# Optimization experiments

Hardware: AMD Instinct MI355X
Metric: run time of the kernel (lower is better)

Reference implementation:

```python
import jax, jax.numpy as jnp
import numpy as np
from jax import lax

SAMPLE_RATE = 0.25
RADIUS = 0.5
NSAMPLE = 32
MLP = [64 + 3, 64, 128]  # use_xyz adds 3 to first width


def setup_inputs() -> dict:
    key = jax.random.key(0)
    ks = jax.random.split(key, 8)
    B, N, C = 8, 8192, 64
    pos = jax.random.normal(ks[0], (B, N, 3), dtype=jnp.float32)
    features = jax.random.normal(ks[1], (B, C, N), dtype=jnp.float32)
    # shared MLP (1x1 Conv2d with bias, ReLU), He-scaled init
    w0 = jax.random.normal(ks[2], (MLP[1], MLP[0]), jnp.float32) * (2.0 / MLP[0]) ** 0.5
    b0 = jnp.zeros((MLP[1],), jnp.float32)
    w1 = jax.random.normal(ks[3], (MLP[1], MLP[1]), jnp.float32) * (2.0 / MLP[1]) ** 0.5
    b1 = jnp.zeros((MLP[1],), jnp.float32)
    w2 = jax.random.normal(ks[4], (MLP[2], MLP[1]), jnp.float32) * (2.0 / MLP[1]) ** 0.5
    b2 = jnp.zeros((MLP[2],), jnp.float32)
    return {"pos": pos, "features": features, "w0": w0, "b0": b0,
            "w1": w1, "b1": b1, "w2": w2, "b2": b2}


def furthest_point_sample(pos, npoint):
    """pos: (B,N,3) -> idx (B,npoint) int32, greedy FPS starting at index 0."""
    B, N, _ = pos.shape
    init_idx = jnp.zeros((B,), jnp.int32)
    init_d = jnp.full((B, N), 1e10, jnp.float32)

    def step(carry, _):
        dists, last = carry
        p_last = jnp.take_along_axis(pos, last[:, None, None], axis=1)  # (B,1,3)
        d = jnp.sum((pos - p_last) ** 2, axis=-1)                        # (B,N)
        dists = jnp.minimum(dists, d)
        nxt = jnp.argmax(dists, axis=-1).astype(jnp.int32)
        return (dists, nxt), nxt

    (_, _), rest = lax.scan(step, (init_d, init_idx), None, length=npoint - 1)
    return jnp.concatenate([init_idx[None, :], rest], axis=0).T  # (B,npoint)


def ball_query(pos, new_xyz, nsample, radius):
    """pos (B,N,3), new_xyz (B,S,3) -> idx (B,S,nsample): first nsample pts
    within radius, padded with the first hit (0 if no hit), as in PointNet2 CUDA."""
    B, N, _ = pos.shape
    d2 = jnp.sum((new_xyz[:, :, None, :] - pos[:, None, :, :]) ** 2, axis=-1)  # (B,S,N)
    cand = jnp.where(d2 < radius * radius,
                     jnp.arange(N, dtype=jnp.int32)[None, None, :], N)
    neg_top, _ = lax.top_k(-cand, nsample)     # smallest nsample indices
    idx = -neg_top                              # ascending index order
    first = idx[..., :1]
    pad = jnp.where(first == N, 0, first)
    return jnp.where(idx == N, pad, idx)


def reference(pos, features, w0, b0, w1, b1, w2, b2):
    B, N, _ = pos.shape
    npoint = int(N * SAMPLE_RATE)
    fps_idx = furthest_point_sample(pos, npoint)                         # (B,S)
    new_xyz = jax.vmap(lambda p, i: p[i])(pos, fps_idx)                  # (B,S,3)

    idx = ball_query(pos, new_xyz, NSAMPLE, RADIUS)                      # (B,S,K)
    grouped_xyz = jax.vmap(lambda p, i: p[i])(pos, idx)                  # (B,S,K,3)
    rel_xyz = grouped_xyz - new_xyz[:, :, None, :]                       # (B,S,K,3)
    grouped_feat = jax.vmap(lambda f, i: f[:, i])(features, idx)         # (B,C,S,K)
    x = jnp.concatenate([rel_xyz.transpose(0, 3, 1, 2), grouped_feat], axis=1)  # (B,3+C,S,K)

    def conv_relu(x, w, b):  # 1x1 conv + bias + ReLU
        y = jnp.einsum('oc,bcsk->bosk', w, x) + b[None, :, None, None]
        return jax.nn.relu(y)

    x = conv_relu(x, w0, b0)
    x = conv_relu(x, w1, b1)
    x = conv_relu(x, w2, b2)
    new_features = jnp.max(x, axis=-1)                                   # (B,mlp[-1],S)
    return new_xyz, new_features
```

## Files before the change

kernel.cpp:

```cpp
#include <hip/hip_runtime.h>

#define NB 8
#define NPTS 8192
#define NC_FEAT 64
#define NS 2048
#define NK 32

__device__ __forceinline__ float d2_ref(float px, float py, float pz,
                                        float qx, float qy, float qz) {
  float dx = __fsub_rn(px, qx);
  float dy = __fsub_rn(py, qy);
  float dz = __fsub_rn(pz, qz);
  return __fadd_rn(__fadd_rn(__fmul_rn(dx, dx), __fmul_rn(dy, dy)),
                   __fmul_rn(dz, dz));
}

#define DPP_KEYMAX(key, ctrl)                                                 \
  {                                                                           \
    unsigned _lo = (unsigned)__builtin_amdgcn_update_dpp(                     \
        0, (int)(unsigned)(key), (ctrl), 0xf, 0xf, true);                     \
    unsigned _hi = (unsigned)__builtin_amdgcn_update_dpp(                     \
        0, (int)(unsigned)((key) >> 32), (ctrl), 0xf, 0xf, true);             \
    unsigned long long _o = ((unsigned long long)_hi << 32) | _lo;            \
    if (_o > (key)) (key) = _o;                                               \
  }

__global__ __launch_bounds__(1024)
void k_fps_tp(const float* __restrict__ pos, const float* __restrict__ feat,
              const float* __restrict__ w0, const float* __restrict__ w1,
              const float* __restrict__ w2,
              float* __restrict__ new_xyz, float* __restrict__ featT,
              float* __restrict__ wT) {
  __shared__ __align__(16) float smem[3 * NPTS + 64];
  const int tid = threadIdx.x;

  if (blockIdx.x < NB) {
    const int b = blockIdx.x;
    float* sx = smem;
    float* sy = smem + NPTS;
    float* sz = smem + 2 * NPTS;
    unsigned long long* rk = (unsigned long long*)(smem + 3 * NPTS);

    const float* p = pos + (size_t)b * NPTS * 3;
    for (int i = tid; i < NPTS; i += 1024) {
      sx[i] = p[3 * i + 0];
      sy[i] = p[3 * i + 1];
      sz[i] = p[3 * i + 2];
    }
    __syncthreads();

    float px[8], py[8], pz[8], dist[8];
#pragma unroll
    for (int j = 0; j < 8; ++j) {
      int idx = tid * 8 + j;
      px[j] = sx[idx]; py[j] = sy[idx]; pz[j] = sz[idx];
      dist[j] = 1e10f;
    }
    if (tid == 0) {
      new_xyz[((size_t)b * NS) * 3 + 0] = sx[0];
      new_xyz[((size_t)b * NS) * 3 + 1] = sy[0];
      new_xyz[((size_t)b * NS) * 3 + 2] = sz[0];
    }

    const int lane = tid & 63;
    const int wave = tid >> 6;
    int last = 0, buf = 0;

    for (int it = 1; it < NS; ++it) {
      float qx = sx[last], qy = sy[last], qz = sz[last];
      float bd = -1.0f;
      int bj = 0;
#pragma unroll
      for (int j = 0; j < 8; ++j) {
        float d = d2_ref(px[j], py[j], pz[j], qx, qy, qz);
        float nd = fminf(dist[j], d);
        dist[j] = nd;
        if (nd > bd) { bd = nd; bj = j; }
      }
      unsigned gidx = (unsigned)(tid * 8 + bj);
      unsigned long long key =
          ((unsigned long long)__float_as_uint(bd) << 32) | (unsigned)~gidx;
      DPP_KEYMAX(key, 0x111);
      DPP_KEYMAX(key, 0x112);
      DPP_KEYMAX(key, 0x114);
      DPP_KEYMAX(key, 0x118);
      DPP_KEYMAX(key, 0x142);
      DPP_KEYMAX(key, 0x143);
      if (lane == 63) rk[buf * 16 + wave] = key;
      __syncthreads();
      key = rk[buf * 16 + (lane & 15)];
      DPP_KEYMAX(key, 0x111);
      DPP_KEYMAX(key, 0x112);
      DPP_KEYMAX(key, 0x114);
      DPP_KEYMAX(key, 0x118);
      int fi = (int)~(unsigned)__builtin_amdgcn_readlane((int)(unsigned)key, 15);
      last = fi;
      buf ^= 1;
      if (tid == 0) {
        new_xyz[((size_t)b * NS + it) * 3 + 0] = sx[fi];
        new_xyz[((size_t)b * NS + it) * 3 + 1] = sy[fi];
        new_xyz[((size_t)b * NS + it) * 3 + 2] = sz[fi];
      }
    }
  } else if (blockIdx.x < NB + NB * (NPTS / 64)) {
    const int t = blockIdx.x - NB;
    const int b = t >> 7;
    const int n0 = (t & 127) << 6;
    float* tile = smem;
    const int col = tid & 63;
    const int r0 = tid >> 6;
#pragma unroll
    for (int q = 0; q < 4; ++q) {
      int c = r0 + q * 16;
      tile[c * 65 + col] = feat[((size_t)b * NC_FEAT + c) * NPTS + n0 + col];
    }
    __syncthreads();
#pragma unroll
    for (int q = 0; q < 4; ++q) {
      int r = r0 + q * 16;
      featT[((size_t)b * NPTS + n0 + r) * 64 + col] = tile[col * 65 + r];
    }
  } else {
    for (int i = tid; i < 67 * 64; i += 1024)
      wT[i] = w0[(i & 63) * 67 + (i >> 6)];
    for (int i = tid; i < 64 * 64; i += 1024)
      wT[67 * 64 + i] = w1[(i & 63) * 64 + (i >> 6)];
    for (int i = tid; i < 64 * 128; i += 1024)
      wT[67 * 64 + 64 * 64 + i] = w2[(i & 127) * 64 + (i >> 7)];
  }
}

__global__ __launch_bounds__(256)
void k_ball(const float* __restrict__ pos, const float* __restrict__ nxyz,
            int* __restrict__ ballidx) {
  const int wid = (blockIdx.x * 256 + threadIdx.x) >> 6;
  const int lane = threadIdx.x & 63;
  const int b = wid >> 11;
  const float qx = nxyz[wid * 3 + 0];
  const float qy = nxyz[wid * 3 + 1];
  const float qz = nxyz[wid * 3 + 2];
  const float* p = pos + (size_t)b * NPTS * 3;
  int* outp = ballidx + (size_t)wid * NK;

  int cnt = 0;
  int firstidx = 0x7fffffff;
  for (int n0 = 0; n0 < NPTS; n0 += 64) {
    const int i = n0 + lane;
    float d2 = d2_ref(p[3 * i], p[3 * i + 1], p[3 * i + 2], qx, qy, qz);
    bool hit = d2 < 0.25f;
    unsigned long long mask = __ballot(hit);
    int pre = __popcll(mask & ((1ull << lane) - 1ull));
    int slot = cnt + pre;
    if (hit && slot < NK) outp[slot] = i;
    if (hit && slot == 0) firstidx = i;
    cnt += __popcll(mask);
    if (cnt >= NK) break;
  }
#pragma unroll
  for (int m = 32; m >= 1; m >>= 1)
    firstidx = min(firstidx, __shfl_xor(firstidx, m, 64));
  int pad = (firstidx == 0x7fffffff) ? 0 : firstidx;
  int start = cnt < NK ? cnt : NK;
  if (lane < NK && lane >= start) outp[lane] = pad;
}

#define MLP_FMA16(wr, xc, acc)                                   \
  _Pragma("unroll") for (int o4 = 0; o4 < 16; ++o4) {            \
    float4 w = (wr)[o4];                                         \
    (acc)[o4 * 4 + 0] = fmaf(w.x, (xc), (acc)[o4 * 4 + 0]);      \
    (acc)[o4 * 4 + 1] = fmaf(w.y, (xc), (acc)[o4 * 4 + 1]);      \
    (acc)[o4 * 4 + 2] = fmaf(w.z, (xc), (acc)[o4 * 4 + 2]);      \
    (acc)[o4 * 4 + 3] = fmaf(w.w, (xc), (acc)[o4 * 4 + 3]);      \
  }

__global__ __launch_bounds__(256)
void k_mlp(const float* __restrict__ pos, const float* __restrict__ featT,
           const float* __restrict__ wT, const float* __restrict__ b0,
           const float* __restrict__ b1, const float* __restrict__ b2,
           const int* __restrict__ ballidx, const float* __restrict__ nxyz,
           float* __restrict__ outf) {
  __shared__ float xs[64 * 256];
  const int tid = threadIdx.x;
  const int g = blockIdx.x * 256 + tid;
  const int s = (g >> 5) & (NS - 1);
  const int b = g >> 16;

  const int idx = ballidx[g];
  const float qx = nxyz[((size_t)b * NS + s) * 3 + 0];
  const float qy = nxyz[((size_t)b * NS + s) * 3 + 1];
  const float qz = nxyz[((size_t)b * NS + s) * 3 + 2];
  const float* pp = pos + ((size_t)b * NPTS + idx) * 3;
  const float x0 = __fsub_rn(pp[0], qx);
  const float x1 = __fsub_rn(pp[1], qy);
  const float x2 = __fsub_rn(pp[2], qz);

  const float4* fT = (const float4*)(featT + ((size_t)b * NPTS + idx) * 64);
#pragma unroll
  for (int c4 = 0; c4 < 16; ++c4) {
    float4 v = fT[c4];
    xs[(c4 * 4 + 0) * 256 + tid] = v.x;
    xs[(c4 * 4 + 1) * 256 + tid] = v.y;
    xs[(c4 * 4 + 2) * 256 + tid] = v.z;
    xs[(c4 * 4 + 3) * 256 + tid] = v.w;
  }

  const float* wt0 = wT;
  const float* wt1 = wT + 67 * 64;
  const float* wt2 = wT + 67 * 64 + 64 * 64;

  float acc[64];
#pragma unroll
  for (int o = 0; o < 64; ++o) acc[o] = b0[o];
  {
    const float xr0 = x0, xr1 = x1, xr2 = x2;
    const float4* wr;
    wr = (const float4*)(wt0 + 0 * 64); MLP_FMA16(wr, xr0, acc);
    wr = (const float4*)(wt0 + 1 * 64); MLP_FMA16(wr, xr1, acc);
    wr = (const float4*)(wt0 + 2 * 64); MLP_FMA16(wr, xr2, acc);
  }
  for (int c = 0; c < 64; ++c) {
    float xc = xs[c * 256 + tid];
    const float4* wr = (const float4*)(wt0 + (3 + c) * 64);
    MLP_FMA16(wr, xc, acc);
  }
#pragma unroll
  for (int o = 0; o < 64; ++o) xs[o * 256 + tid] = fmaxf(acc[o], 0.0f);

#pragma unroll
  for (int o = 0; o < 64; ++o) acc[o] = b1[o];
  for (int c = 0; c < 64; ++c) {
    float xc = xs[c * 256 + tid];
    const float4* wr = (const float4*)(wt1 + c * 64);
    MLP_FMA16(wr, xc, acc);
  }
#pragma unroll
  for (int o = 0; o < 64; ++o) xs[o * 256 + tid] = fmaxf(acc[o], 0.0f);

#pragma unroll
  for (int h = 0; h < 2; ++h) {
#pragma unroll
    for (int o = 0; o < 64; ++o) acc[o] = b2[h * 64 + o];
    for (int c = 0; c < 64; ++c) {
      float xc = xs[c * 256 + tid];
      const float4* wr = (const float4*)(wt2 + c * 128 + h * 64);
      MLP_FMA16(wr, xc, acc);
    }
#pragma unroll
    for (int o = 0; o < 64; ++o) {
      float v = fmaxf(acc[o], 0.0f);
      v = fmaxf(v, __shfl_xor(v, 16, 64));
      v = fmaxf(v, __shfl_xor(v, 8, 64));
      v = fmaxf(v, __shfl_xor(v, 4, 64));
      v = fmaxf(v, __shfl_xor(v, 2, 64));
      v = fmaxf(v, __shfl_xor(v, 1, 64));
      if ((tid & 31) == 0)
        outf[((size_t)b * 128 + h * 64 + o) * NS + s] = v;
    }
  }
}

extern "C" void kernel_launch(void* const* d_in, const int* in_sizes, int n_in,
                              void* d_out, int out_size, void* d_ws,
                              size_t ws_size, hipStream_t stream) {
  const float* pos = (const float*)d_in[0];
  const float* feat = (const float*)d_in[1];
  const float* w0 = (const float*)d_in[2];
  const float* b0 = (const float*)d_in[3];
  const float* w1 = (const float*)d_in[4];
  const float* b1 = (const float*)d_in[5];
  const float* w2 = (const float*)d_in[6];
  const float* b2 = (const float*)d_in[7];

  float* out = (float*)d_out;
  float* new_xyz = out;
  float* new_feat = out + (size_t)NB * NS * 3;

  int* ballidx = (int*)d_ws;
  float* featT = (float*)d_ws + (size_t)NB * NS * NK;
  float* wT = featT + (size_t)NB * NPTS * 64;

  hipLaunchKernelGGL(k_fps_tp, dim3(NB + NB * (NPTS / 64) + 1), dim3(1024), 0,
                     stream, pos, feat, w0, w1, w2, new_xyz, featT, wT);
  hipLaunchKernelGGL(k_ball, dim3((NB * NS) / 4), dim3(256), 0, stream, pos,
                     new_xyz, ballidx);
  hipLaunchKernelGGL(k_mlp, dim3((NB * NS * NK) / 256), dim3(256), 0, stream,
                     pos, featT, wT, b0, b1, b2, ballidx, new_xyz, new_feat);
}
```

Before: 2.588 ms.

## Split FPS from transpose, use 512 threads with packed v2f distance updates

```diff
diff --git a/kernel.cpp b/kernel.cpp
--- a/kernel.cpp
+++ b/kernel.cpp
@@ -5,6 +5,8 @@
 #define NC_FEAT 64
 #define NS 2048
 #define NK 32
+
+typedef float v2f __attribute__((ext_vector_type(2)));
 
 __device__ __forceinline__ float d2_ref(float px, float py, float pz,
                                         float qx, float qy, float qz) {
@@ -25,107 +27,126 @@
     if (_o > (key)) (key) = _o;                                               \
   }
 
-__global__ __launch_bounds__(1024)
-void k_fps_tp(const float* __restrict__ pos, const float* __restrict__ feat,
-              const float* __restrict__ w0, const float* __restrict__ w1,
-              const float* __restrict__ w2,
-              float* __restrict__ new_xyz, float* __restrict__ featT,
-              float* __restrict__ wT) {
+__global__ __launch_bounds__(512)
+void k_fps(const float* __restrict__ pos, float* __restrict__ new_xyz) {
+#pragma clang fp contract(off)
   __shared__ __align__(16) float smem[3 * NPTS + 64];
   const int tid = threadIdx.x;
-
-  if (blockIdx.x < NB) {
-    const int b = blockIdx.x;
-    float* sx = smem;
-    float* sy = smem + NPTS;
-    float* sz = smem + 2 * NPTS;
-    unsigned long long* rk = (unsigned long long*)(smem + 3 * NPTS);
-
-    const float* p = pos + (size_t)b * NPTS * 3;
-    for (int i = tid; i < NPTS; i += 1024) {
-      sx[i] = p[3 * i + 0];
-      sy[i] = p[3 * i + 1];
-      sz[i] = p[3 * i + 2];
-    }
+  const int b = blockIdx.x;
+  float* sx = smem;
+  float* sy = smem + NPTS;
+  float* sz = smem + 2 * NPTS;
+  unsigned long long* rk = (unsigned long long*)(smem + 3 * NPTS);
+
+  const float* p = pos + (size_t)b * NPTS * 3;
+  for (int i = tid; i < NPTS; i += 512) {
+    sx[i] = p[3 * i + 0];
+    sy[i] = p[3 * i + 1];
+    sz[i] = p[3 * i + 2];
+  }
+  if (tid < 32) rk[tid] = 0ull;
+  __syncthreads();
+
+  const int base = tid * 16;
+  v2f px[8], py[8], pz[8], di[8];
+#pragma unroll
+  for (int k = 0; k < 8; ++k) {
+    px[k] = (v2f){sx[base + 2 * k], sx[base + 2 * k + 1]};
+    py[k] = (v2f){sy[base + 2 * k], sy[base + 2 * k + 1]};
+    pz[k] = (v2f){sz[base + 2 * k], sz[base + 2 * k + 1]};
+    di[k] = (v2f){1e10f, 1e10f};
+  }
+  if (tid == 0) {
+    new_xyz[((size_t)b * NS) * 3 + 0] = sx[0];
+    new_xyz[((size_t)b * NS) * 3 + 1] = sy[0];
+    new_xyz[((size_t)b * NS) * 3 + 2] = sz[0];
+  }
+
+  const int lane = tid & 63;
+  const int wave = tid >> 6;
+  const unsigned nbase = ~(unsigned)base;
+  int last = 0, buf = 0;
+
+  for (int it = 1; it < NS; ++it) {
+    float qx = sx[last], qy = sy[last], qz = sz[last];
+#pragma unroll
+    for (int k = 0; k < 8; ++k) {
+      v2f dx = px[k] - qx;
+      v2f dy = py[k] - qy;
+      v2f dz = pz[k] - qz;
+      v2f d2 = (dx * dx + dy * dy) + dz * dz;
+      di[k] = __builtin_elementwise_min(di[k], d2);
+    }
+    v2f m0 = __builtin_elementwise_max(di[0], di[1]);
+    v2f m1 = __builtin_elementwise_max(di[2], di[3]);
+    v2f m2 = __builtin_elementwise_max(di[4], di[5]);
+    v2f m3 = __builtin_elementwise_max(di[6], di[7]);
+    v2f m4 = __builtin_elementwise_max(m0, m1);
+    v2f m5 = __builtin_elementwise_max(m2, m3);
+    v2f m6 = __builtin_elementwise_max(m4, m5);
+    float bd = fmaxf(m6.x, m6.y);
+    int bj = 0;
+#pragma unroll
+    for (int j = 15; j >= 0; --j) {
+      float v = (j & 1) ? di[j >> 1].y : di[j >> 1].x;
+      if (v == bd) bj = j;
+    }
+    unsigned long long key =
+        ((unsigned long long)__float_as_uint(bd) << 32) |
+        (unsigned)(nbase - (unsigned)bj);
+    DPP_KEYMAX(key, 0x111);
+    DPP_KEYMAX(key, 0x112);
+    DPP_KEYMAX(key, 0x114);
+    DPP_KEYMAX(key, 0x118);
+    DPP_KEYMAX(key, 0x142);
+    DPP_KEYMAX(key, 0x143);
+    if (lane == 63) rk[buf * 16 + wave] = key;
     __syncthreads();
-
-    float px[8], py[8], pz[8], dist[8];
-#pragma unroll
-    for (int j = 0; j < 8; ++j) {
-      int idx = tid * 8 + j;
-      px[j] = sx[idx]; py[j] = sy[idx]; pz[j] = sz[idx];
-      dist[j] = 1e10f;
-    }
+    key = rk[buf * 16 + (lane & 15)];
+    DPP_KEYMAX(key, 0x111);
+    DPP_KEYMAX(key, 0x112);
+    DPP_KEYMAX(key, 0x114);
+    DPP_KEYMAX(key, 0x118);
+    int fi = (int)~(unsigned)__builtin_amdgcn_readlane((int)(unsigned)key, 15);
+    last = fi;
+    buf ^= 1;
     if (tid == 0) {
-      new_xyz[((size_t)b * NS) * 3 + 0] = sx[0];
-      new_xyz[((size_t)b * NS) * 3 + 1] = sy[0];
-      new_xyz[((size_t)b * NS) * 3 + 2] = sz[0];
-    }
-
-    const int lane = tid & 63;
-    const int wave = tid >> 6;
-    int last = 0, buf = 0;
-
-    for (int it = 1; it < NS; ++it) {
-      float qx = sx[last], qy = sy[last], qz = sz[last];
-      float bd = -1.0f;
-      int bj = 0;
-#pragma unroll
-      for (int j = 0; j < 8; ++j) {
-        float d = d2_ref(px[j], py[j], pz[j], qx, qy, qz);
-        float nd = fminf(dist[j], d);
-        dist[j] = nd;
-        if (nd > bd) { bd = nd; bj = j; }
-      }
-      unsigned gidx = (unsigned)(tid * 8 + bj);
-      unsigned long long key =
-          ((unsigned long long)__float_as_uint(bd) << 32) | (unsigned)~gidx;
-      DPP_KEYMAX(key, 0x111);
-      DPP_KEYMAX(key, 0x112);
-      DPP_KEYMAX(key, 0x114);
-      DPP_KEYMAX(key, 0x118);
-      DPP_KEYMAX(key, 0x142);
-      DPP_KEYMAX(key, 0x143);
-      if (lane == 63) rk[buf * 16 + wave] = key;
-      __syncthreads();
-      key = rk[buf * 16 + (lane & 15)];
-      DPP_KEYMAX(key, 0x111);
-      DPP_KEYMAX(key, 0x112);
-      DPP_KEYMAX(key, 0x114);
-      DPP_KEYMAX(key, 0x118);
-      int fi = (int)~(unsigned)__builtin_amdgcn_readlane((int)(unsigned)key, 15);
-      last = fi;
-      buf ^= 1;
-      if (tid == 0) {
-        new_xyz[((size_t)b * NS + it) * 3 + 0] = sx[fi];
-        new_xyz[((size_t)b * NS + it) * 3 + 1] = sy[fi];
-        new_xyz[((size_t)b * NS + it) * 3 + 2] = sz[fi];
-      }
-    }
-  } else if (blockIdx.x < NB + NB * (NPTS / 64)) {
-    const int t = blockIdx.x - NB;
+      new_xyz[((size_t)b * NS + it) * 3 + 0] = sx[fi];
+      new_xyz[((size_t)b * NS + it) * 3 + 1] = sy[fi];
+      new_xyz[((size_t)b * NS + it) * 3 + 2] = sz[fi];
+    }
+  }
+}
+
+__global__ __launch_bounds__(256)
+void k_tp(const float* __restrict__ feat, const float* __restrict__ w0,
+          const float* __restrict__ w1, const float* __restrict__ w2,
+          float* __restrict__ featT, float* __restrict__ wT) {
+  __shared__ float tile[64 * 65];
+  const int tid = threadIdx.x;
+  if (blockIdx.x < NB * (NPTS / 64)) {
+    const int t = blockIdx.x;
     const int b = t >> 7;
     const int n0 = (t & 127) << 6;
-    float* tile = smem;
     const int col = tid & 63;
     const int r0 = tid >> 6;
 #pragma unroll
-    for (int q = 0; q < 4; ++q) {
-      int c = r0 + q * 16;
+    for (int q = 0; q < 16; ++q) {
+      int c = r0 + q * 4;
       tile[c * 65 + col] = feat[((size_t)b * NC_FEAT + c) * NPTS + n0 + col];
     }
     __syncthreads();
 #pragma unroll
-    for (int q = 0; q < 4; ++q) {
-      int r = r0 + q * 16;
+    for (int q = 0; q < 16; ++q) {
+      int r = r0 + q * 4;
       featT[((size_t)b * NPTS + n0 + r) * 64 + col] = tile[col * 65 + r];
     }
   } else {
-    for (int i = tid; i < 67 * 64; i += 1024)
+    for (int i = tid; i < 67 * 64; i += 256)
       wT[i] = w0[(i & 63) * 67 + (i >> 6)];
-    for (int i = tid; i < 64 * 64; i += 1024)
+    for (int i = tid; i < 64 * 64; i += 256)
       wT[67 * 64 + i] = w1[(i & 63) * 64 + (i >> 6)];
-    for (int i = tid; i < 64 * 128; i += 1024)
+    for (int i = tid; i < 64 * 128; i += 256)
       wT[67 * 64 + 64 * 64 + i] = w2[(i & 127) * 64 + (i >> 7)];
   }
 }
@@ -279,8 +300,9 @@
   float* featT = (float*)d_ws + (size_t)NB * NS * NK;
   float* wT = featT + (size_t)NB * NPTS * 64;
 
-  hipLaunchKernelGGL(k_fps_tp, dim3(NB + NB * (NPTS / 64) + 1), dim3(1024), 0,
-                     stream, pos, feat, w0, w1, w2, new_xyz, featT, wT);
+  hipLaunchKernelGGL(k_tp, dim3(NB * (NPTS / 64) + 1), dim3(256), 0, stream,
+                     feat, w0, w1, w2, featT, wT);
+  hipLaunchKernelGGL(k_fps, dim3(NB), dim3(512), 0, stream, pos, new_xyz);
   hipLaunchKernelGGL(k_ball, dim3((NB * NS) / 4), dim3(256), 0, stream, pos,
                      new_xyz, ballidx);
   hipLaunchKernelGGL(k_mlp, dim3((NB * NS * NK) / 256), dim3(256), 0, stream,
```

New measurement: 2.457 ms. 1.05x faster.
